# Kernel optimization log

Measured on AMD Instinct MI355X. Metric: run time of the kernel, lower is better.

## Reference

```python
import jax, jax.numpy as jnp
import numpy as np

EPS = 1e-6
TEMPERATURE = 1.0


def setup_inputs() -> dict:
    key = jax.random.key(0)
    ks = jax.random.split(key, 8)
    B, N, T, H, NH = 128, 16, 32, 128, 4
    L = (N + 1) * T
    node_enc = jax.random.normal(ks[0], (B, T, H), dtype=jnp.float32)
    neigh_enc = jax.random.normal(ks[1], (B, N, T, H), dtype=jnp.float32)
    attn_mask = jax.random.randint(ks[2], (B, L), 0, 2).astype(bool)
    attn_mask = attn_mask.at[:, 0].set(False)  # ensure no fully-masked row
    w_qs = jax.random.normal(ks[3], (NH, H, H), dtype=jnp.float32) * 0.05
    w_ks = jax.random.normal(ks[4], (NH, H, H), dtype=jnp.float32) * 0.05
    w_vs = jax.random.normal(ks[5], (NH, H, H), dtype=jnp.float32) * 0.05
    prj_w = jax.random.normal(ks[6], (H, NH * H), dtype=jnp.float32) * 0.05
    prj_b = jnp.zeros((H,), dtype=jnp.float32)
    ln_gamma = jnp.ones((H,), dtype=jnp.float32)
    ln_beta = jnp.zeros((H,), dtype=jnp.float32)
    return {"node_enc": node_enc, "neigh_enc": neigh_enc, "attn_mask": attn_mask,
            "current_time_step": 5, "w_qs": w_qs, "w_ks": w_ks, "w_vs": w_vs,
            "prj_w": prj_w, "prj_b": prj_b, "ln_gamma": ln_gamma, "ln_beta": ln_beta}


def reference(node_enc, neigh_enc, attn_mask, current_time_step,
              w_qs, w_ks, w_vs, prj_w, prj_b, ln_gamma, ln_beta):
    B, T, H = node_enc.shape
    N = neigh_enc.shape[1]
    NH = w_qs.shape[0]
    q = node_enc[:, current_time_step]                       # [B, H]
    # split(neigh_enc,1,dim=1) + cat(dim=2) == reshape to [B, N*T, H]
    kv = jnp.concatenate([node_enc, neigh_enc.reshape(B, N * T, H)], axis=1)  # [B, L, H]
    q_s = jnp.einsum('bh,nhd->nbd', q, w_qs)                 # [NH, B, H]
    k_s = jnp.einsum('blh,nhd->nbld', kv, w_ks)              # [NH, B, L, H]
    v_s = jnp.einsum('blh,nhd->nbld', kv, w_vs)              # [NH, B, L, H]
    S = jnp.einsum('nbd,nbld->nbl', q_s, k_s)                # [NH, B, L]
    S = jnp.where(attn_mask[None, :, :], -jnp.inf, S)
    S = S / (TEMPERATURE * jnp.sqrt(jnp.float32(H)))
    A = jax.nn.softmax(S, axis=-1)                           # [NH, B, L]
    ctx = jnp.einsum('nbl,nbld->nbd', A, v_s)                # [NH, B, H]
    # torch cat of head-splits along dim=-1 -> [B, NH*H], head-major
    cat = jnp.transpose(ctx, (1, 0, 2)).reshape(B, NH * H)
    proj = cat @ prj_w.T + prj_b                             # [B, H]
    x = proj + q
    mean = jnp.mean(x, axis=-1, keepdims=True)
    var = jnp.var(x, axis=-1, keepdims=True)
    out = (x - mean) / jnp.sqrt(var + EPS) * ln_gamma + ln_beta
    slf_attn = jnp.sum(A, axis=0)[:, None, :]                # [B, 1, L]
    return (out, slf_attn)
```

## Files before the change

kernel.cpp:

```cpp
#include <hip/hip_runtime.h>

#define B_  128
#define N_  16
#define T_  32
#define H_  128
#define NH_ 4
#define L_  544

__device__ __forceinline__ float wave_reduce_sum(float v) {
    #pragma unroll
    for (int off = 32; off > 0; off >>= 1) v += __shfl_xor(v, off, 64);
    return v;
}
__device__ __forceinline__ float wave_reduce_max(float v) {
    #pragma unroll
    for (int off = 32; off > 0; off >>= 1) v = fmaxf(v, __shfl_xor(v, off, 64));
    return v;
}

__global__ __launch_bounds__(256) void attn_kernel(
    const float* __restrict__ node_enc, const float* __restrict__ neigh_enc,
    const int* __restrict__ attn_mask, const int* __restrict__ cts_p,
    const float* __restrict__ w_qs, const float* __restrict__ w_ks,
    float* __restrict__ A_ws, float* __restrict__ wctx_ws)
{
    const int bid  = blockIdx.x;
    const int b    = bid >> 1;
    const int pair = bid & 1;
    const int n0   = pair * 2;
    const int t    = threadIdx.x;
    const int cts  = cts_p[0];

    __shared__ __align__(16) float q_sh[H_];
    __shared__ __align__(16) float qs_sh[2][H_];
    __shared__ __align__(16) float qk_sh[2][H_];
    __shared__ __align__(16) float S_sh[2][L_ + 4];
    __shared__ float red_sh[2][2];

    if (t < H_) q_sh[t] = node_enc[b * (T_ * H_) + cts * H_ + t];
    __syncthreads();

    {
        int g = t >> 7, d = t & 127;
        const float* w = w_qs + (n0 + g) * (H_ * H_) + d;
        float acc = 0.f;
        #pragma unroll 8
        for (int h = 0; h < H_; ++h) acc += q_sh[h] * w[h * H_];
        qs_sh[g][d] = acc;
    }
    __syncthreads();

    {
        int g = t >> 7, h = t & 127;
        const float4* w = (const float4*)(w_ks + (n0 + g) * (H_ * H_) + h * H_);
        const float* qs = qs_sh[g];
        float acc = 0.f;
        #pragma unroll 8
        for (int d4 = 0; d4 < H_ / 4; ++d4) {
            float4 v = w[d4];
            acc += v.x * qs[d4 * 4] + v.y * qs[d4 * 4 + 1]
                 + v.z * qs[d4 * 4 + 2] + v.w * qs[d4 * 4 + 3];
        }
        qk_sh[g][h] = acc;
    }
    __syncthreads();

    const float scale = 0.08838834764831845f;
    for (int l = t; l < L_; l += 256) {
        const float* rowp = (l < T_)
            ? node_enc  + (size_t)b * (T_ * H_) + l * H_
            : neigh_enc + (size_t)b * (N_ * T_ * H_) + (l - T_) * H_;
        const float4* row = (const float4*)rowp;
        float a0 = 0.f, a1 = 0.f;
        #pragma unroll
        for (int h4 = 0; h4 < H_ / 4; ++h4) {
            float4 v = row[h4];
            int h = h4 * 4;
            a0 += v.x * qk_sh[0][h] + v.y * qk_sh[0][h + 1]
                + v.z * qk_sh[0][h + 2] + v.w * qk_sh[0][h + 3];
            a1 += v.x * qk_sh[1][h] + v.y * qk_sh[1][h + 1]
                + v.z * qk_sh[1][h + 2] + v.w * qk_sh[1][h + 3];
        }
        int m = attn_mask[b * L_ + l];
        S_sh[0][l] = m ? -__builtin_inff() : a0 * scale;
        S_sh[1][l] = m ? -__builtin_inff() : a1 * scale;
    }
    __syncthreads();

    {
        int g = t >> 7, j = t & 127;
        int wv = (t >> 6) & 1;
        float m = -__builtin_inff();
        for (int l = j; l < L_; l += 128) m = fmaxf(m, S_sh[g][l]);
        m = wave_reduce_max(m);
        if ((t & 63) == 0) red_sh[g][wv] = m;
        __syncthreads();
        float mfin = fmaxf(red_sh[g][0], red_sh[g][1]);
        float s = 0.f;
        for (int l = j; l < L_; l += 128) {
            float e = __expf(S_sh[g][l] - mfin);
            S_sh[g][l] = e;
            s += e;
        }
        s = wave_reduce_sum(s);
        __syncthreads();
        if ((t & 63) == 0) red_sh[g][wv] = s;
        __syncthreads();
        float inv = 1.0f / (red_sh[g][0] + red_sh[g][1]);
        for (int l = j; l < L_; l += 128) {
            float a = S_sh[g][l] * inv;
            S_sh[g][l] = a;
            A_ws[(size_t)(n0 + g) * (B_ * L_) + b * L_ + l] = a;
        }
    }
    __syncthreads();

    {
        int g = t >> 7, h = t & 127;
        const float* As = S_sh[g];
        float acc = 0.f;
        const float* base0 = node_enc + (size_t)b * (T_ * H_) + h;
        #pragma unroll 8
        for (int l = 0; l < T_; ++l) acc += As[l] * base0[l * H_];
        const float* base1 = neigh_enc + (size_t)b * (N_ * T_ * H_) + h;
        #pragma unroll 8
        for (int l = 0; l < L_ - T_; ++l) acc += As[T_ + l] * base1[l * H_];
        wctx_ws[(size_t)(n0 + g) * (B_ * H_) + b * H_ + h] = acc;
    }
}

__global__ __launch_bounds__(256) void finish_kernel(
    const float* __restrict__ node_enc, const int* __restrict__ cts_p,
    const float* __restrict__ w_vs, const float* __restrict__ prj_w,
    const float* __restrict__ prj_b, const float* __restrict__ ln_gamma,
    const float* __restrict__ ln_beta, const float* __restrict__ A_ws,
    const float* __restrict__ wctx_ws, float* __restrict__ d_out)
{
    const int b = blockIdx.x;
    const int t = threadIdx.x;
    __shared__ __align__(16) float wctx_sh[NH_ * H_];
    __shared__ __align__(16) float ctx_sh[NH_ * H_];
    __shared__ __align__(16) float part_sh[256];
    __shared__ __align__(16) float x_sh[H_];
    __shared__ float stat_sh[2];

    float* slf = d_out + B_ * H_;
    for (int l = t; l < L_; l += 256) {
        float s = 0.f;
        #pragma unroll
        for (int n = 0; n < NH_; ++n) s += A_ws[(size_t)n * (B_ * L_) + b * L_ + l];
        slf[b * L_ + l] = s;
    }
    for (int idx = t; idx < NH_ * H_; idx += 256) {
        int n = idx >> 7, h = idx & 127;
        wctx_sh[idx] = wctx_ws[(size_t)n * (B_ * H_) + b * H_ + h];
    }
    __syncthreads();
    for (int idx = t; idx < NH_ * H_; idx += 256) {
        int n = idx >> 7, d = idx & 127;
        const float* w  = w_vs + (size_t)n * (H_ * H_) + d;
        const float* wc = wctx_sh + n * H_;
        float acc = 0.f;
        #pragma unroll 8
        for (int h = 0; h < H_; ++h) acc += wc[h] * w[h * H_];
        ctx_sh[idx] = acc;
    }
    __syncthreads();
    {
        int j = t >> 1, half = t & 1;
        const float4* w = (const float4*)(prj_w + (size_t)j * (NH_ * H_) + half * 256);
        const float4* c = (const float4*)(ctx_sh + half * 256);
        float acc = 0.f;
        #pragma unroll 8
        for (int i = 0; i < 64; ++i) {
            float4 wv = w[i]; float4 cv = c[i];
            acc += wv.x * cv.x + wv.y * cv.y + wv.z * cv.z + wv.w * cv.w;
        }
        part_sh[t] = acc;
    }
    __syncthreads();
    const int cts = cts_p[0];
    if (t < H_) {
        float x = part_sh[2 * t] + part_sh[2 * t + 1] + prj_b[t]
                + node_enc[(size_t)b * (T_ * H_) + cts * H_ + t];
        x_sh[t] = x;
    }
    __syncthreads();
    if (t < 64) {
        float v0 = x_sh[t], v1 = x_sh[t + 64];
        float s1 = v0 + v1;
        float s2 = v0 * v0 + v1 * v1;
        s1 = wave_reduce_sum(s1);
        s2 = wave_reduce_sum(s2);
        if (t == 0) {
            float mean = s1 / (float)H_;
            float var  = s2 / (float)H_ - mean * mean;
            stat_sh[0] = mean;
            stat_sh[1] = rsqrtf(var + 1e-6f);
        }
    }
    __syncthreads();
    if (t < H_) {
        float y = (x_sh[t] - stat_sh[0]) * stat_sh[1] * ln_gamma[t] + ln_beta[t];
        d_out[b * H_ + t] = y;
    }
}

extern "C" void kernel_launch(void* const* d_in, const int* in_sizes, int n_in,
                              void* d_out, int out_size, void* d_ws, size_t ws_size,
                              hipStream_t stream) {
    const float* node_enc  = (const float*)d_in[0];
    const float* neigh_enc = (const float*)d_in[1];
    const int*   attn_mask = (const int*)d_in[2];
    const int*   cts       = (const int*)d_in[3];
    const float* w_qs      = (const float*)d_in[4];
    const float* w_ks      = (const float*)d_in[5];
    const float* w_vs      = (const float*)d_in[6];
    const float* prj_w     = (const float*)d_in[7];
    const float* prj_b     = (const float*)d_in[8];
    const float* ln_gamma  = (const float*)d_in[9];
    const float* ln_beta   = (const float*)d_in[10];

    float* A_ws    = (float*)d_ws;
    float* wctx_ws = A_ws + (size_t)NH_ * B_ * L_;

    attn_kernel<<<B_ * 2, 256, 0, stream>>>(node_enc, neigh_enc, attn_mask, cts,
                                            w_qs, w_ks, A_ws, wctx_ws);
    finish_kernel<<<B_, 256, 0, stream>>>(node_enc, cts, w_vs, prj_w, prj_b,
                                          ln_gamma, ln_beta, A_ws, wctx_ws,
                                          (float*)d_out);
}
```

Baseline: 153.8 us.

## Split attention over L into chunks with flash-style partial softmax merge

Computes the q·Wq·Wk projection in its own kernel. The main attention pass is then split across 9 chunks of 64 keys per batch, giving 1152 blocks instead of 256. Each chunk stages its K/V rows in shared memory once, computes scores for all 4 heads, and emits a local max, sum and weighted partial context. The finish kernel merges these with rescaling and rebuilds the summed attention weights from the stored scores. This targets low occupancy and the repeated global reads of the encodings, at the cost of an extra launch and more workspace traffic.

```diff
diff --git a/kernel.cpp b/kernel.cpp
--- a/kernel.cpp
+++ b/kernel.cpp
@@ -6,204 +6,245 @@
 #define H_  128
 #define NH_ 4
 #define L_  544
-
-__device__ __forceinline__ float wave_reduce_sum(float v) {
-    #pragma unroll
-    for (int off = 32; off > 0; off >>= 1) v += __shfl_xor(v, off, 64);
-    return v;
-}
-__device__ __forceinline__ float wave_reduce_max(float v) {
-    #pragma unroll
-    for (int off = 32; off > 0; off >>= 1) v = fmaxf(v, __shfl_xor(v, off, 64));
-    return v;
-}
-
-__global__ __launch_bounds__(256) void attn_kernel(
+#define CH  64
+#define NC  9
+
+__global__ __launch_bounds__(256) void qk_kernel(
+    const float* __restrict__ node_enc, const int* __restrict__ cts_p,
+    const float* __restrict__ w_qs, const float* __restrict__ w_ks,
+    float* __restrict__ qk_ws)
+{
+    const int blk = blockIdx.x;
+    const int b = blk & 127, n = blk >> 7;
+    const int t = threadIdx.x;
+    __shared__ float q_sh[H_];
+    __shared__ float ps[256];
+    __shared__ float qs_sh[H_];
+
+    if (t < H_) q_sh[t] = node_enc[(size_t)b*T_*H_ + cts_p[0]*H_ + t];
+    __syncthreads();
+    {
+        int d = t & 127, half = t >> 7;
+        const float* w  = w_qs + (size_t)n*H_*H_ + (half*64)*H_ + d;
+        const float* qh = q_sh + half*64;
+        float acc = 0.f;
+        #pragma unroll 8
+        for (int h = 0; h < 64; ++h) acc += qh[h] * w[h*H_];
+        ps[t] = acc;
+    }
+    __syncthreads();
+    if (t < H_) qs_sh[t] = ps[t] + ps[t+128];
+    __syncthreads();
+    {
+        int h = t & 127, half = t >> 7;
+        const float4* w  = (const float4*)(w_ks + (size_t)n*H_*H_ + h*H_ + half*64);
+        const float4* qs = (const float4*)(qs_sh + half*64);
+        float acc = 0.f;
+        #pragma unroll
+        for (int i = 0; i < 16; ++i) {
+            float4 wv = w[i], qv = qs[i];
+            acc += wv.x*qv.x + wv.y*qv.y + wv.z*qv.z + wv.w*qv.w;
+        }
+        ps[t] = acc;
+    }
+    __syncthreads();
+    if (t < H_) qk_ws[(b*NH_ + n)*H_ + t] = ps[t] + ps[t+128];
+}
+
+__global__ __launch_bounds__(256) void attn_main_kernel(
     const float* __restrict__ node_enc, const float* __restrict__ neigh_enc,
-    const int* __restrict__ attn_mask, const int* __restrict__ cts_p,
-    const float* __restrict__ w_qs, const float* __restrict__ w_ks,
-    float* __restrict__ A_ws, float* __restrict__ wctx_ws)
+    const int* __restrict__ attn_mask, const float* __restrict__ qk_ws,
+    float* __restrict__ S_ws, float* __restrict__ wpart_ws,
+    float* __restrict__ stats_ws)
 {
-    const int bid  = blockIdx.x;
-    const int b    = bid >> 1;
-    const int pair = bid & 1;
-    const int n0   = pair * 2;
-    const int t    = threadIdx.x;
-    const int cts  = cts_p[0];
-
-    __shared__ __align__(16) float q_sh[H_];
-    __shared__ __align__(16) float qs_sh[2][H_];
-    __shared__ __align__(16) float qk_sh[2][H_];
-    __shared__ __align__(16) float S_sh[2][L_ + 4];
-    __shared__ float red_sh[2][2];
-
-    if (t < H_) q_sh[t] = node_enc[b * (T_ * H_) + cts * H_ + t];
-    __syncthreads();
-
-    {
-        int g = t >> 7, d = t & 127;
-        const float* w = w_qs + (n0 + g) * (H_ * H_) + d;
-        float acc = 0.f;
-        #pragma unroll 8
-        for (int h = 0; h < H_; ++h) acc += q_sh[h] * w[h * H_];
-        qs_sh[g][d] = acc;
-    }
-    __syncthreads();
-
-    {
-        int g = t >> 7, h = t & 127;
-        const float4* w = (const float4*)(w_ks + (n0 + g) * (H_ * H_) + h * H_);
-        const float* qs = qs_sh[g];
-        float acc = 0.f;
-        #pragma unroll 8
-        for (int d4 = 0; d4 < H_ / 4; ++d4) {
-            float4 v = w[d4];
-            acc += v.x * qs[d4 * 4] + v.y * qs[d4 * 4 + 1]
-                 + v.z * qs[d4 * 4 + 2] + v.w * qs[d4 * 4 + 3];
-        }
-        qk_sh[g][h] = acc;
-    }
-    __syncthreads();
-
-    const float scale = 0.08838834764831845f;
-    for (int l = t; l < L_; l += 256) {
+    const int blk = blockIdx.x;
+    const int b = blk / NC, c = blk % NC;
+    const int t = threadIdx.x;
+    const int l0 = c * CH;
+    const int R  = min(CH, L_ - l0);
+
+    __shared__ __align__(16) float kv_sh[CH*132];
+    __shared__ __align__(16) float qk_sh[4*132];
+    __shared__ float S_sh[CH*5];
+    __shared__ float P_sh[CH*6];
+    __shared__ int   msk_sh[CH];
+
+    for (int j = t; j < 4*H_; j += 256) {
+        int g = j >> 7, h = j & 127;
+        qk_sh[g*132 + h] = qk_ws[(b*NH_ + g)*H_ + h];
+    }
+    if (t < R) msk_sh[t] = attn_mask[b*L_ + l0 + t];
+    for (int j = t; j < R*32; j += 256) {
+        int r = j >> 5, cc = j & 31;
+        int l = l0 + r;
         const float* rowp = (l < T_)
-            ? node_enc  + (size_t)b * (T_ * H_) + l * H_
-            : neigh_enc + (size_t)b * (N_ * T_ * H_) + (l - T_) * H_;
-        const float4* row = (const float4*)rowp;
-        float a0 = 0.f, a1 = 0.f;
-        #pragma unroll
-        for (int h4 = 0; h4 < H_ / 4; ++h4) {
-            float4 v = row[h4];
-            int h = h4 * 4;
-            a0 += v.x * qk_sh[0][h] + v.y * qk_sh[0][h + 1]
-                + v.z * qk_sh[0][h + 2] + v.w * qk_sh[0][h + 3];
-            a1 += v.x * qk_sh[1][h] + v.y * qk_sh[1][h + 1]
-                + v.z * qk_sh[1][h + 2] + v.w * qk_sh[1][h + 3];
-        }
-        int m = attn_mask[b * L_ + l];
-        S_sh[0][l] = m ? -__builtin_inff() : a0 * scale;
-        S_sh[1][l] = m ? -__builtin_inff() : a1 * scale;
-    }
-    __syncthreads();
-
-    {
-        int g = t >> 7, j = t & 127;
-        int wv = (t >> 6) & 1;
-        float m = -__builtin_inff();
-        for (int l = j; l < L_; l += 128) m = fmaxf(m, S_sh[g][l]);
-        m = wave_reduce_max(m);
-        if ((t & 63) == 0) red_sh[g][wv] = m;
-        __syncthreads();
-        float mfin = fmaxf(red_sh[g][0], red_sh[g][1]);
-        float s = 0.f;
-        for (int l = j; l < L_; l += 128) {
-            float e = __expf(S_sh[g][l] - mfin);
-            S_sh[g][l] = e;
-            s += e;
-        }
-        s = wave_reduce_sum(s);
-        __syncthreads();
-        if ((t & 63) == 0) red_sh[g][wv] = s;
-        __syncthreads();
-        float inv = 1.0f / (red_sh[g][0] + red_sh[g][1]);
-        for (int l = j; l < L_; l += 128) {
-            float a = S_sh[g][l] * inv;
-            S_sh[g][l] = a;
-            A_ws[(size_t)(n0 + g) * (B_ * L_) + b * L_ + l] = a;
-        }
-    }
-    __syncthreads();
-
-    {
-        int g = t >> 7, h = t & 127;
-        const float* As = S_sh[g];
-        float acc = 0.f;
-        const float* base0 = node_enc + (size_t)b * (T_ * H_) + h;
-        #pragma unroll 8
-        for (int l = 0; l < T_; ++l) acc += As[l] * base0[l * H_];
-        const float* base1 = neigh_enc + (size_t)b * (N_ * T_ * H_) + h;
-        #pragma unroll 8
-        for (int l = 0; l < L_ - T_; ++l) acc += As[T_ + l] * base1[l * H_];
-        wctx_ws[(size_t)(n0 + g) * (B_ * H_) + b * H_ + h] = acc;
-    }
-}
-
-__global__ __launch_bounds__(256) void finish_kernel(
+            ? node_enc  + (size_t)b*T_*H_ + l*H_
+            : neigh_enc + (size_t)b*N_*T_*H_ + (size_t)(l - T_)*H_;
+        float4 v = ((const float4*)rowp)[cc];
+        *((float4*)(kv_sh + r*132 + cc*4)) = v;
+    }
+    __syncthreads();
+
+    {
+        int r = t >> 2, g = t & 3;
+        float S = -INFINITY;
+        if (r < R) {
+            const float4* kvv = (const float4*)(kv_sh + r*132);
+            const float4* qv  = (const float4*)(qk_sh + g*132);
+            float acc = 0.f;
+            #pragma unroll
+            for (int i = 0; i < 32; ++i) {
+                float4 a = kvv[i], q = qv[i];
+                acc += a.x*q.x + a.y*q.y + a.z*q.z + a.w*q.w;
+            }
+            S = msk_sh[r] ? -INFINITY : acc * 0.08838834764831845f;
+            S_ws[((size_t)b*L_ + l0 + r)*NH_ + g] = S;
+        }
+        S_sh[r*5 + g] = S;
+    }
+    __syncthreads();
+
+    {
+        int w = t >> 6, lane = t & 63;
+        float v = S_sh[lane*5 + w];
+        float m = v;
+        #pragma unroll
+        for (int off = 32; off > 0; off >>= 1) m = fmaxf(m, __shfl_xor(m, off, 64));
+        m = fmaxf(m, -1e30f);
+        float p = __expf(v - m);
+        P_sh[lane*6 + w] = p;
+        float s = p;
+        #pragma unroll
+        for (int off = 32; off > 0; off >>= 1) s += __shfl_xor(s, off, 64);
+        if (lane == 0) {
+            stats_ws[((b*NC + c)*NH_ + w)*2 + 0] = m;
+            stats_ws[((b*NC + c)*NH_ + w)*2 + 1] = s;
+        }
+    }
+    __syncthreads();
+
+    {
+        int h = t & 127, gp = t >> 7;
+        float acc0 = 0.f, acc1 = 0.f;
+        #pragma unroll 4
+        for (int r = 0; r < R; ++r) {
+            float  kvv = kv_sh[r*132 + h];
+            float2 p = *((const float2*)(P_sh + r*6 + gp*2));
+            acc0 += p.x * kvv;
+            acc1 += p.y * kvv;
+        }
+        float* wp = wpart_ws + (size_t)(b*NC + c)*NH_*H_;
+        wp[(gp*2+0)*H_ + h] = acc0;
+        wp[(gp*2+1)*H_ + h] = acc1;
+    }
+}
+
+__global__ __launch_bounds__(512) void finish_kernel(
     const float* __restrict__ node_enc, const int* __restrict__ cts_p,
     const float* __restrict__ w_vs, const float* __restrict__ prj_w,
     const float* __restrict__ prj_b, const float* __restrict__ ln_gamma,
-    const float* __restrict__ ln_beta, const float* __restrict__ A_ws,
-    const float* __restrict__ wctx_ws, float* __restrict__ d_out)
+    const float* __restrict__ ln_beta, const float* __restrict__ S_ws,
+    const float* __restrict__ wpart_ws, const float* __restrict__ stats_ws,
+    float* __restrict__ d_out)
 {
-    const int b = blockIdx.x;
-    const int t = threadIdx.x;
-    __shared__ __align__(16) float wctx_sh[NH_ * H_];
-    __shared__ __align__(16) float ctx_sh[NH_ * H_];
-    __shared__ __align__(16) float part_sh[256];
-    __shared__ __align__(16) float x_sh[H_];
-    __shared__ float stat_sh[2];
-
-    float* slf = d_out + B_ * H_;
-    for (int l = t; l < L_; l += 256) {
+    const int b = blockIdx.x, t = threadIdx.x;
+    __shared__ float stats_sh[NC*NH_*2];
+    __shared__ float m_sh[NH_], inv_sh[NH_];
+    __shared__ float scale_sh[NC*NH_];
+    __shared__ __align__(16) float wctx_sh[NH_*H_];
+    __shared__ __align__(16) float cat_sh[NH_*H_];
+    __shared__ float part_sh[512];
+    __shared__ float x_sh[H_];
+    __shared__ float st2[2];
+
+    if (t < NC*NH_*2) stats_sh[t] = stats_ws[b*NC*NH_*2 + t];
+    __syncthreads();
+    if (t < NH_) {
+        float m = -INFINITY;
+        #pragma unroll
+        for (int c = 0; c < NC; ++c) m = fmaxf(m, stats_sh[(c*NH_+t)*2]);
         float s = 0.f;
         #pragma unroll
-        for (int n = 0; n < NH_; ++n) s += A_ws[(size_t)n * (B_ * L_) + b * L_ + l];
-        slf[b * L_ + l] = s;
-    }
-    for (int idx = t; idx < NH_ * H_; idx += 256) {
-        int n = idx >> 7, h = idx & 127;
-        wctx_sh[idx] = wctx_ws[(size_t)n * (B_ * H_) + b * H_ + h];
-    }
-    __syncthreads();
-    for (int idx = t; idx < NH_ * H_; idx += 256) {
-        int n = idx >> 7, d = idx & 127;
-        const float* w  = w_vs + (size_t)n * (H_ * H_) + d;
-        const float* wc = wctx_sh + n * H_;
+        for (int c = 0; c < NC; ++c)
+            s += stats_sh[(c*NH_+t)*2+1] * __expf(stats_sh[(c*NH_+t)*2] - m);
+        m_sh[t] = m;
+        inv_sh[t] = 1.0f / s;
+    }
+    __syncthreads();
+    if (t < NC*NH_) {
+        int c = t >> 2, n = t & 3;
+        scale_sh[t] = __expf(stats_sh[(c*NH_+n)*2] - m_sh[n]) * inv_sh[n];
+    }
+    __syncthreads();
+
+    {
+        float m0 = m_sh[0], m1 = m_sh[1], m2 = m_sh[2], m3 = m_sh[3];
+        float i0 = inv_sh[0], i1 = inv_sh[1], i2 = inv_sh[2], i3 = inv_sh[3];
+        float* slf = d_out + B_*H_ + b*L_;
+        const float4* Sr = (const float4*)(S_ws + (size_t)b*L_*NH_);
+        for (int l = t; l < L_; l += 512) {
+            float4 s4 = Sr[l];
+            slf[l] = __expf(s4.x - m0)*i0 + __expf(s4.y - m1)*i1
+                   + __expf(s4.z - m2)*i2 + __expf(s4.w - m3)*i3;
+        }
+    }
+    {
+        int n = t >> 7;
+        const float* wp = wpart_ws + (size_t)b*NC*NH_*H_;
+        float acc = 0.f;
+        #pragma unroll
+        for (int c = 0; c < NC; ++c)
+            acc += wp[c*NH_*H_ + t] * scale_sh[c*NH_ + n];
+        wctx_sh[t] = acc;
+    }
+    __syncthreads();
+    {
+        int n = t >> 7, d = t & 127;
+        const float* w  = w_vs + (size_t)n*H_*H_ + d;
+        const float* wc = wctx_sh + n*H_;
         float acc = 0.f;
         #pragma unroll 8
-        for (int h = 0; h < H_; ++h) acc += wc[h] * w[h * H_];
-        ctx_sh[idx] = acc;
-    }
-    __syncthreads();
-    {
-        int j = t >> 1, half = t & 1;
-        const float4* w = (const float4*)(prj_w + (size_t)j * (NH_ * H_) + half * 256);
-        const float4* c = (const float4*)(ctx_sh + half * 256);
-        float acc = 0.f;
-        #pragma unroll 8
-        for (int i = 0; i < 64; ++i) {
-            float4 wv = w[i]; float4 cv = c[i];
-            acc += wv.x * cv.x + wv.y * cv.y + wv.z * cv.z + wv.w * cv.w;
+        for (int h = 0; h < H_; ++h) acc += wc[h] * w[h*H_];
+        cat_sh[t] = acc;
+    }
+    __syncthreads();
+    {
+        int j = t >> 2, q = t & 3;
+        const float4* w  = (const float4*)(prj_w + (size_t)j*(NH_*H_) + q*128);
+        const float4* cc = (const float4*)(cat_sh + q*128);
+        float acc = 0.f;
+        #pragma unroll
+        for (int i = 0; i < 32; ++i) {
+            float4 wv = w[i], cv = cc[i];
+            acc += wv.x*cv.x + wv.y*cv.y + wv.z*cv.z + wv.w*cv.w;
         }
         part_sh[t] = acc;
     }
     __syncthreads();
-    const int cts = cts_p[0];
     if (t < H_) {
-        float x = part_sh[2 * t] + part_sh[2 * t + 1] + prj_b[t]
-                + node_enc[(size_t)b * (T_ * H_) + cts * H_ + t];
+        float x = part_sh[4*t] + part_sh[4*t+1] + part_sh[4*t+2] + part_sh[4*t+3]
+                + prj_b[t] + node_enc[(size_t)b*T_*H_ + cts_p[0]*H_ + t];
         x_sh[t] = x;
     }
     __syncthreads();
     if (t < 64) {
-        float v0 = x_sh[t], v1 = x_sh[t + 64];
-        float s1 = v0 + v1;
-        float s2 = v0 * v0 + v1 * v1;
-        s1 = wave_reduce_sum(s1);
-        s2 = wave_reduce_sum(s2);
+        float v0 = x_sh[t], v1 = x_sh[t+64];
+        float s1 = v0 + v1, s2 = v0*v0 + v1*v1;
+        #pragma unroll
+        for (int off = 32; off > 0; off >>= 1) {
+            s1 += __shfl_xor(s1, off, 64);
+            s2 += __shfl_xor(s2, off, 64);
+        }
         if (t == 0) {
             float mean = s1 / (float)H_;
-            float var  = s2 / (float)H_ - mean * mean;
-            stat_sh[0] = mean;
-            stat_sh[1] = rsqrtf(var + 1e-6f);
-        }
-    }
-    __syncthreads();
-    if (t < H_) {
-        float y = (x_sh[t] - stat_sh[0]) * stat_sh[1] * ln_gamma[t] + ln_beta[t];
-        d_out[b * H_ + t] = y;
-    }
+            float var  = s2 / (float)H_ - mean*mean;
+            st2[0] = mean;
+            st2[1] = rsqrtf(var + 1e-6f);
+        }
+    }
+    __syncthreads();
+    if (t < H_)
+        d_out[b*H_ + t] = (x_sh[t] - st2[0]) * st2[1] * ln_gamma[t] + ln_beta[t];
 }
 
 extern "C" void kernel_launch(void* const* d_in, const int* in_sizes, int n_in,
@@ -221,12 +262,15 @@
     const float* ln_gamma  = (const float*)d_in[9];
     const float* ln_beta   = (const float*)d_in[10];
 
-    float* A_ws    = (float*)d_ws;
-    float* wctx_ws = A_ws + (size_t)NH_ * B_ * L_;
-
-    attn_kernel<<<B_ * 2, 256, 0, stream>>>(node_enc, neigh_enc, attn_mask, cts,
-                                            w_qs, w_ks, A_ws, wctx_ws);
-    finish_kernel<<<B_, 256, 0, stream>>>(node_enc, cts, w_vs, prj_w, prj_b,
-                                          ln_gamma, ln_beta, A_ws, wctx_ws,
-                                          (float*)d_out);
-}
+    float* qk_ws    = (float*)d_ws;
+    float* S_ws     = qk_ws + (size_t)B_*NH_*H_;
+    float* wpart_ws = S_ws + (size_t)B_*L_*NH_;
+    float* stats_ws = wpart_ws + (size_t)B_*NC*NH_*H_;
+
+    qk_kernel<<<B_*NH_, 256, 0, stream>>>(node_enc, cts, w_qs, w_ks, qk_ws);
+    attn_main_kernel<<<B_*NC, 256, 0, stream>>>(node_enc, neigh_enc, attn_mask,
+                                                qk_ws, S_ws, wpart_ws, stats_ws);
+    finish_kernel<<<B_, 512, 0, stream>>>(node_enc, cts, w_vs, prj_w, prj_b,
+                                          ln_gamma, ln_beta, S_ws, wpart_ws,
+                                          stats_ws, (float*)d_out);
+}
```

Measured after the change: 129.7 us. 15.6% less time.
